# Optimization experiments

Measured on AMD Instinct MI355X. Metric: run time of the kernel, lower is better.

Reference implementation:

```python
import jax, jax.numpy as jnp
import numpy as np

N_NODES = 100000
N_EDGES = 3200000
OUT_CH = 128
X_DIM = 128


def setup_inputs() -> dict:
    key = jax.random.key(0)
    k1, k2, k3, k4 = jax.random.split(key, 4)
    x = jax.random.normal(k1, (N_NODES, X_DIM), dtype=jnp.float32)
    edge_index = jax.random.randint(k2, (2, N_EDGES), 0, N_NODES, dtype=jnp.int64)
    # torch nn.Linear(num_nodes, out_channels): weight [out, N], bias [out]
    W_weight = jax.random.normal(k3, (OUT_CH, N_NODES), dtype=jnp.float32) * (1.0 / np.sqrt(N_NODES))
    W_bias = jax.random.normal(k4, (OUT_CH,), dtype=jnp.float32) * 0.01
    return {"x": x, "edge_index": edge_index, "W_weight": W_weight, "W_bias": W_bias}


def reference(x, edge_index, W_weight, W_bias):
    """LINK forward: logits = A @ W.T + b, A = sparse COO adjacency from edge_index.

    A[r, c] = 1 for each edge (r, c), so row r of the output is
    sum_{c in neighbors(r)} W.T[c] + b  -> gather + segment_sum (SpMM).
    """
    N = x.shape[0]
    row, col = edge_index[0], edge_index[1]
    Wt = W_weight.T  # [N, out]
    gathered = Wt[col]  # [E, out] irregular gather
    logits = jax.ops.segment_sum(gathered, row, num_segments=N) + W_bias  # [N, out]
    return logits
```

## Files before the change

kernel.cpp:

```cpp
#include <hip/hip_runtime.h>
#include <hip/hip_bf16.h>


#define NCHUNK 256
#define RPB7 128
#define NB7 782
#define CAP 5120

__global__ __launch_bounds__(256) void absmax_kernel(const float* __restrict__ W,
                                                     int n4,
                                                     unsigned int* __restrict__ amax) {
    int i = blockIdx.x * blockDim.x + threadIdx.x;
    int stride = gridDim.x * blockDim.x;
    float m = 0.f;
    const float4* W4 = (const float4*)W;
    for (; i < n4; i += stride) {
        float4 v = W4[i];
        m = fmaxf(m, fmaxf(fmaxf(fabsf(v.x), fabsf(v.y)),
                           fmaxf(fabsf(v.z), fabsf(v.w))));
    }
    for (int off = 32; off > 0; off >>= 1) m = fmaxf(m, __shfl_xor(m, off));
    if ((threadIdx.x & 63) == 0) atomicMax(amax, __float_as_uint(m));
}

__global__ __launch_bounds__(256) void quant_kernel(const float* __restrict__ W,
                                                    unsigned char* __restrict__ Wt8,
                                                    const unsigned int* __restrict__ amax,
                                                    int N) {
    __shared__ float tile[128][33];
    int cx = threadIdx.x;
    int oy = threadIdx.y;
    int c = blockIdx.x * 32 + cx;
    for (int k = 0; k < 16; ++k) {
        int o = oy * 16 + k;
        tile[o][cx] = (c < N) ? W[(size_t)o * N + c] : 0.f;
    }
    __syncthreads();
    float M = __uint_as_float(*amax);
    float si = (M > 0.f) ? 127.f / M : 0.f;
    if (c < N) {
        unsigned int w[4];
#pragma unroll
        for (int d = 0; d < 4; ++d) {
            unsigned int acc = 0;
#pragma unroll
            for (int b = 0; b < 4; ++b) {
                int o = oy * 16 + d * 4 + b;
                int qi = __float2int_rn(tile[o][cx] * si) + 128;
                acc |= ((unsigned int)(qi & 0xff)) << (8 * b);
            }
            w[d] = acc;
        }
        *(uint4*)(Wt8 + (size_t)c * 128 + oy * 16) =
            make_uint4(w[0], w[1], w[2], w[3]);
    }
}

__global__ __launch_bounds__(1024) void p1_hist(const int* __restrict__ row,
                                                int E, int* __restrict__ hist) {
    __shared__ int lh[NB7];
    int b = blockIdx.x;
    for (int k = threadIdx.x; k < NB7; k += blockDim.x) lh[k] = 0;
    __syncthreads();
    int ch = (E + NCHUNK - 1) / NCHUNK;
    int s = b * ch, e = min(E, s + ch);
    for (int i = s + threadIdx.x; i < e; i += blockDim.x)
        atomicAdd(&lh[row[i] >> 7], 1);
    __syncthreads();
    for (int k = threadIdx.x; k < NB7; k += blockDim.x)
        hist[k * NCHUNK + b] = lh[k];
}

__global__ __launch_bounds__(256) void scan_sums(const int* __restrict__ v,
                                                 int* __restrict__ bsums, int M) {
    __shared__ int s[256];
    int i = blockIdx.x * 256 + threadIdx.x;
    s[threadIdx.x] = (i < M) ? v[i] : 0;
    __syncthreads();
    for (int off = 128; off > 0; off >>= 1) {
        if (threadIdx.x < off) s[threadIdx.x] += s[threadIdx.x + off];
        __syncthreads();
    }
    if (threadIdx.x == 0) bsums[blockIdx.x] = s[0];
}

__global__ __launch_bounds__(256) void scan_offsets_par(int* __restrict__ bsums,
                                                        int nb) {
    __shared__ int s[256];
    __shared__ int carry;
    if (threadIdx.x == 0) carry = 0;
    __syncthreads();
    for (int base = 0; base < nb; base += 256) {
        int i = base + threadIdx.x;
        int v = (i < nb) ? bsums[i] : 0;
        s[threadIdx.x] = v;
        __syncthreads();
        for (int off = 1; off < 256; off <<= 1) {
            int t = (threadIdx.x >= off) ? s[threadIdx.x - off] : 0;
            __syncthreads();
            s[threadIdx.x] += t;
            __syncthreads();
        }
        int incl = s[threadIdx.x];
        int c = carry;
        __syncthreads();
        if (threadIdx.x == 255) carry = c + incl;
        if (i < nb) bsums[i] = c + incl - v;
        __syncthreads();
    }
}

__global__ __launch_bounds__(256) void scan_finalT(const int* __restrict__ hist,
                                                   const int* __restrict__ bsums,
                                                   int* __restrict__ S_T,
                                                   int* __restrict__ bstart,
                                                   int M) {
    __shared__ int s[256];
    int i = blockIdx.x * 256 + threadIdx.x;
    int x = (i < M) ? hist[i] : 0;
    s[threadIdx.x] = x;
    __syncthreads();
    for (int off = 1; off < 256; off <<= 1) {
        int t = (threadIdx.x >= off) ? s[threadIdx.x - off] : 0;
        __syncthreads();
        s[threadIdx.x] += t;
        __syncthreads();
    }
    if (i < M) {
        int val = bsums[blockIdx.x] + s[threadIdx.x] - x;
        int k = i >> 8;
        int b = i & (NCHUNK - 1);
        S_T[(size_t)b * NB7 + k] = val;
        if (b == 0) bstart[k] = val;
    }
}

__global__ __launch_bounds__(1024) void p1_scatter(const int* __restrict__ row,
                                                   const int* __restrict__ col,
                                                   int E,
                                                   const int* __restrict__ S_T,
                                                   unsigned* __restrict__ packed) {
    __shared__ int lc[NB7];
    int b = blockIdx.x;
    const int* Srow = S_T + (size_t)b * NB7;
    for (int k = threadIdx.x; k < NB7; k += blockDim.x) lc[k] = Srow[k];
    __syncthreads();
    int ch = (E + NCHUNK - 1) / NCHUNK;
    int s = b * ch, e = min(E, s + ch);
    for (int i = s + threadIdx.x; i < e; i += blockDim.x) {
        int r = row[i], c = col[i];
        int p = atomicAdd(&lc[r >> 7], 1);
        packed[p] = ((unsigned)(r & 127) << 17) | (unsigned)c;
    }
}

__global__ __launch_bounds__(1024) void spmm_fused(
    const unsigned* __restrict__ packed, const int* __restrict__ bstart,
    const unsigned char* __restrict__ Wt8, const float* __restrict__ bias,
    const unsigned int* __restrict__ amax, float* __restrict__ out, int E,
    int N) {
    __shared__ unsigned g2[CAP];
    __shared__ int rhist[RPB7];
    __shared__ int rs[RPB7 + 1];
    __shared__ int cursor[RPB7];
    __shared__ int sscan[RPB7];
    int k = blockIdx.x;
    int start = bstart[k];
    int end = (k + 1 < NB7) ? bstart[k + 1] : E;
    int cnt = end - start;
    if (cnt > CAP) cnt = CAP;

    int tid = threadIdx.x;
    if (tid < RPB7) rhist[tid] = 0;
    __syncthreads();

    unsigned st0 = 0, st1 = 0, st2 = 0, st3 = 0, st4 = 0;
    {
        int i;
        i = tid;
        if (i < cnt) { st0 = packed[start + i]; atomicAdd(&rhist[st0 >> 17], 1); }
        i = tid + 1024;
        if (i < cnt) { st1 = packed[start + i]; atomicAdd(&rhist[st1 >> 17], 1); }
        i = tid + 2048;
        if (i < cnt) { st2 = packed[start + i]; atomicAdd(&rhist[st2 >> 17], 1); }
        i = tid + 3072;
        if (i < cnt) { st3 = packed[start + i]; atomicAdd(&rhist[st3 >> 17], 1); }
        i = tid + 4096;
        if (i < cnt) { st4 = packed[start + i]; atomicAdd(&rhist[st4 >> 17], 1); }
    }
    __syncthreads();
    {
        int v = 0;
        if (tid < RPB7) { v = rhist[tid]; sscan[tid] = v; }
        __syncthreads();
        for (int off = 1; off < RPB7; off <<= 1) {
            int t = 0;
            if (tid < RPB7 && tid >= off) t = sscan[tid - off];
            __syncthreads();
            if (tid < RPB7 && tid >= off) sscan[tid] += t;
            __syncthreads();
        }
        if (tid < RPB7) {
            rs[tid] = sscan[tid] - v;
            cursor[tid] = sscan[tid] - v;
            if (tid == RPB7 - 1) rs[RPB7] = sscan[RPB7 - 1];
        }
    }
    __syncthreads();
    {
        int i;
        i = tid;
        if (i < cnt) { int p = atomicAdd(&cursor[st0 >> 17], 1); g2[p] = (st0 & 0x1FFFFu) << 7; }
        i = tid + 1024;
        if (i < cnt) { int p = atomicAdd(&cursor[st1 >> 17], 1); g2[p] = (st1 & 0x1FFFFu) << 7; }
        i = tid + 2048;
        if (i < cnt) { int p = atomicAdd(&cursor[st2 >> 17], 1); g2[p] = (st2 & 0x1FFFFu) << 7; }
        i = tid + 3072;
        if (i < cnt) { int p = atomicAdd(&cursor[st3 >> 17], 1); g2[p] = (st3 & 0x1FFFFu) << 7; }
        i = tid + 4096;
        if (i < cnt) { int p = atomicAdd(&cursor[st4 >> 17], 1); g2[p] = (st4 & 0x1FFFFu) << 7; }
    }
    __syncthreads();

    float sg = __uint_as_float(*amax) / 127.f;
    int wave = tid >> 6, lane = tid & 63;
    int h = lane >> 5;
    int lane4 = (lane & 31) * 4;

    for (int ri = 0; ri < 8; ++ri) {
        int r = wave * 8 + ri;
        int gr = k * RPB7 + r;
        int js = rs[r], je = rs[r + 1];
        int m = je - js;
        int T = m >> 1;
        unsigned accA = 0, accB = 0;
        int idx = js + h;
        int t = 0;
        for (; t + 4 <= T; t += 4) {
            unsigned e0 = g2[idx + 0];
            unsigned e1 = g2[idx + 2];
            unsigned e2 = g2[idx + 4];
            unsigned e3 = g2[idx + 6];
            idx += 8;
            uint32_t u0 = *(const uint32_t*)(Wt8 + e0 + lane4);
            uint32_t u1 = *(const uint32_t*)(Wt8 + e1 + lane4);
            uint32_t u2 = *(const uint32_t*)(Wt8 + e2 + lane4);
            uint32_t u3 = *(const uint32_t*)(Wt8 + e3 + lane4);
            accA += (u0 & 0x00FF00FFu);
            accB += ((u0 >> 8) & 0x00FF00FFu);
            accA += (u1 & 0x00FF00FFu);
            accB += ((u1 >> 8) & 0x00FF00FFu);
            accA += (u2 & 0x00FF00FFu);
            accB += ((u2 >> 8) & 0x00FF00FFu);
            accA += (u3 & 0x00FF00FFu);
            accB += ((u3 >> 8) & 0x00FF00FFu);
        }
        for (; t < T; ++t) {
            unsigned e0 = g2[idx];
            idx += 2;
            uint32_t u0 = *(const uint32_t*)(Wt8 + e0 + lane4);
            accA += (u0 & 0x00FF00FFu);
            accB += ((u0 >> 8) & 0x00FF00FFu);
        }
        if ((m & 1) && h == 0) {
            unsigned e0 = g2[je - 1];
            uint32_t u0 = *(const uint32_t*)(Wt8 + e0 + lane4);
            accA += (u0 & 0x00FF00FFu);
            accB += ((u0 >> 8) & 0x00FF00FFu);
        }
        accA += __shfl_xor(accA, 32);
        accB += __shfl_xor(accB, 32);
        if (h == 0 && gr < N) {
            float fm = -128.f * (float)m;
            float4 b4 = *(const float4*)(bias + lane4);
            float4 res;
            res.x = fmaf(sg, (float)(accA & 0xffffu) + fm, b4.x);
            res.y = fmaf(sg, (float)(accB & 0xffffu) + fm, b4.y);
            res.z = fmaf(sg, (float)(accA >> 16) + fm, b4.z);
            res.w = fmaf(sg, (float)(accB >> 16) + fm, b4.w);
            *(float4*)(out + (size_t)gr * 128 + lane4) = res;
        }
    }
}

extern "C" void kernel_launch(void* const* d_in, const int* in_sizes, int n_in,
                              void* d_out, int out_size, void* d_ws,
                              size_t ws_size, hipStream_t stream) {
    const int* edge = (const int*)d_in[1];
    const float* W = (const float*)d_in[2];
    const float* bias = (const float*)d_in[3];
    float* out = (float*)d_out;

    const int N = in_sizes[0] / 128;
    const int E = in_sizes[1] / 2;
    const int* row = edge;
    const int* col = edge + E;

    const int M = NB7 * NCHUNK;
    const int nb1 = (M + 255) / 256;

    auto align16 = [](size_t v) { return (v + 15) & ~(size_t)15; };
    char* ws = (char*)d_ws;
    size_t off = 0;
    unsigned char* Wt8 = (unsigned char*)(ws + off);
    off = align16(off + (size_t)N * 128);
    unsigned* packed = (unsigned*)(ws + off);
    off = align16(off + (size_t)E * sizeof(unsigned));
    int* hist = (int*)(ws + off);
    off = align16(off + (size_t)M * sizeof(int));
    int* S_T = (int*)(ws + off);
    off = align16(off + (size_t)M * sizeof(int));
    int* bs1 = (int*)(ws + off);
    off = align16(off + (size_t)nb1 * sizeof(int));
    int* bstart = (int*)(ws + off);
    off = align16(off + (size_t)(NB7 + 1) * sizeof(int));
    unsigned int* amax = (unsigned int*)(ws + off);
    off = align16(off + 16);

    hipMemsetAsync(amax, 0, sizeof(unsigned int), stream);

    absmax_kernel<<<1024, 256, 0, stream>>>(W, (128 * N) / 4, amax);
    {
        dim3 block(32, 8);
        dim3 grid((N + 31) / 32);
        quant_kernel<<<grid, block, 0, stream>>>(W, Wt8, amax, N);
    }
    p1_hist<<<NCHUNK, 1024, 0, stream>>>(row, E, hist);
    scan_sums<<<nb1, 256, 0, stream>>>(hist, bs1, M);
    scan_offsets_par<<<1, 256, 0, stream>>>(bs1, nb1);
    scan_finalT<<<nb1, 256, 0, stream>>>(hist, bs1, S_T, bstart, M);
    p1_scatter<<<NCHUNK, 1024, 0, stream>>>(row, col, E, S_T, packed);
    spmm_fused<<<NB7, 1024, 0, stream>>>(packed, bstart, Wt8, bias, amax, out,
                                         E, N);
}
```

Measured before the change: 189.5 us.

## Split fused bin-sort SpMM into global row-sort pass and fine-grained gather kernel

The single fused kernel, which sorted each 128-row bin in shared memory and then gathered, is replaced by two kernels. A row-sort pass over coarser 512-row bins writes a full CSR (row starts plus column offsets) to global memory. A separate gather kernel with small 256-thread blocks then walks each row, broadcasting column indices across the wave with shuffles. The aim is higher occupancy and better latency hiding in the gather, and removing the shared-memory CAP limit. The cost is an extra kernel launch and an extra global write and read of the edge array.

New measurement: 204.0 us. 1.08x slower.

```diff
diff --git a/kernel.cpp b/kernel.cpp
--- a/kernel.cpp
+++ b/kernel.cpp
@@ -3,9 +3,8 @@
 
 
 #define NCHUNK 256
-#define RPB7 128
-#define NB7 782
-#define CAP 5120
+#define BINROWS 512
+#define NBIN 196
 
 __global__ __launch_bounds__(256) void absmax_kernel(const float* __restrict__ W,
                                                      int n4,
@@ -58,16 +57,16 @@
 
 __global__ __launch_bounds__(1024) void p1_hist(const int* __restrict__ row,
                                                 int E, int* __restrict__ hist) {
-    __shared__ int lh[NB7];
+    __shared__ int lh[NBIN];
     int b = blockIdx.x;
-    for (int k = threadIdx.x; k < NB7; k += blockDim.x) lh[k] = 0;
+    for (int k = threadIdx.x; k < NBIN; k += blockDim.x) lh[k] = 0;
     __syncthreads();
     int ch = (E + NCHUNK - 1) / NCHUNK;
     int s = b * ch, e = min(E, s + ch);
     for (int i = s + threadIdx.x; i < e; i += blockDim.x)
-        atomicAdd(&lh[row[i] >> 7], 1);
-    __syncthreads();
-    for (int k = threadIdx.x; k < NB7; k += blockDim.x)
+        atomicAdd(&lh[row[i] >> 9], 1);
+    __syncthreads();
+    for (int k = threadIdx.x; k < NBIN; k += blockDim.x)
         hist[k * NCHUNK + b] = lh[k];
 }
 
@@ -113,7 +112,7 @@
 __global__ __launch_bounds__(256) void scan_finalT(const int* __restrict__ hist,
                                                    const int* __restrict__ bsums,
                                                    int* __restrict__ S_T,
-                                                   int* __restrict__ bstart,
+                                                   int* __restrict__ binstart,
                                                    int M) {
     __shared__ int s[256];
     int i = blockIdx.x * 256 + threadIdx.x;
@@ -130,8 +129,8 @@
         int val = bsums[blockIdx.x] + s[threadIdx.x] - x;
         int k = i >> 8;
         int b = i & (NCHUNK - 1);
-        S_T[(size_t)b * NB7 + k] = val;
-        if (b == 0) bstart[k] = val;
+        S_T[(size_t)b * NBIN + k] = val;
+        if (b == 0) binstart[k] = val;
     }
 }
 
@@ -140,137 +139,108 @@
                                                    int E,
                                                    const int* __restrict__ S_T,
                                                    unsigned* __restrict__ packed) {
-    __shared__ int lc[NB7];
+    __shared__ int lc[NBIN];
     int b = blockIdx.x;
-    const int* Srow = S_T + (size_t)b * NB7;
-    for (int k = threadIdx.x; k < NB7; k += blockDim.x) lc[k] = Srow[k];
+    const int* Srow = S_T + (size_t)b * NBIN;
+    for (int k = threadIdx.x; k < NBIN; k += blockDim.x) lc[k] = Srow[k];
     __syncthreads();
     int ch = (E + NCHUNK - 1) / NCHUNK;
     int s = b * ch, e = min(E, s + ch);
     for (int i = s + threadIdx.x; i < e; i += blockDim.x) {
         int r = row[i], c = col[i];
-        int p = atomicAdd(&lc[r >> 7], 1);
-        packed[p] = ((unsigned)(r & 127) << 17) | (unsigned)c;
-    }
-}
-
-__global__ __launch_bounds__(1024) void spmm_fused(
-    const unsigned* __restrict__ packed, const int* __restrict__ bstart,
+        int p = atomicAdd(&lc[r >> 9], 1);
+        packed[p] = ((unsigned)(r & 511) << 17) | (unsigned)c;
+    }
+}
+
+__global__ __launch_bounds__(1024) void p2_rowsort(const unsigned* __restrict__ packed,
+                                                   const int* __restrict__ binstart,
+                                                   unsigned* __restrict__ colsorted,
+                                                   int* __restrict__ rowstart,
+                                                   int E) {
+    __shared__ int lh[BINROWS];
+    __shared__ int sc[BINROWS];
+    __shared__ int cur[BINROWS];
+    int b = blockIdx.x;
+    int tid = threadIdx.x;
+    int start = binstart[b];
+    int end = (b + 1 < NBIN) ? binstart[b + 1] : E;
+    if (tid < BINROWS) lh[tid] = 0;
+    __syncthreads();
+    for (int i = start + tid; i < end; i += 1024)
+        atomicAdd(&lh[packed[i] >> 17], 1);
+    __syncthreads();
+    int v = 0;
+    if (tid < BINROWS) { v = lh[tid]; sc[tid] = v; }
+    __syncthreads();
+    for (int off = 1; off < BINROWS; off <<= 1) {
+        int t = 0;
+        if (tid < BINROWS && tid >= off) t = sc[tid - off];
+        __syncthreads();
+        if (tid < BINROWS && tid >= off) sc[tid] += t;
+        __syncthreads();
+    }
+    if (tid < BINROWS) {
+        int excl = sc[tid] - v;
+        rowstart[b * BINROWS + tid] = start + excl;
+        cur[tid] = start + excl;
+    }
+    __syncthreads();
+    for (int i = start + tid; i < end; i += 1024) {
+        unsigned e2 = packed[i];
+        int p = atomicAdd(&cur[e2 >> 17], 1);
+        colsorted[p] = (e2 & 0x1FFFFu) << 7;
+    }
+}
+
+__global__ __launch_bounds__(256, 8) void spmm_gather(
+    const unsigned* __restrict__ colsorted, const int* __restrict__ rowstart,
     const unsigned char* __restrict__ Wt8, const float* __restrict__ bias,
-    const unsigned int* __restrict__ amax, float* __restrict__ out, int E,
-    int N) {
-    __shared__ unsigned g2[CAP];
-    __shared__ int rhist[RPB7];
-    __shared__ int rs[RPB7 + 1];
-    __shared__ int cursor[RPB7];
-    __shared__ int sscan[RPB7];
-    int k = blockIdx.x;
-    int start = bstart[k];
-    int end = (k + 1 < NB7) ? bstart[k + 1] : E;
-    int cnt = end - start;
-    if (cnt > CAP) cnt = CAP;
-
-    int tid = threadIdx.x;
-    if (tid < RPB7) rhist[tid] = 0;
-    __syncthreads();
-
-    unsigned st0 = 0, st1 = 0, st2 = 0, st3 = 0, st4 = 0;
-    {
-        int i;
-        i = tid;
-        if (i < cnt) { st0 = packed[start + i]; atomicAdd(&rhist[st0 >> 17], 1); }
-        i = tid + 1024;
-        if (i < cnt) { st1 = packed[start + i]; atomicAdd(&rhist[st1 >> 17], 1); }
-        i = tid + 2048;
-        if (i < cnt) { st2 = packed[start + i]; atomicAdd(&rhist[st2 >> 17], 1); }
-        i = tid + 3072;
-        if (i < cnt) { st3 = packed[start + i]; atomicAdd(&rhist[st3 >> 17], 1); }
-        i = tid + 4096;
-        if (i < cnt) { st4 = packed[start + i]; atomicAdd(&rhist[st4 >> 17], 1); }
-    }
-    __syncthreads();
-    {
-        int v = 0;
-        if (tid < RPB7) { v = rhist[tid]; sscan[tid] = v; }
-        __syncthreads();
-        for (int off = 1; off < RPB7; off <<= 1) {
-            int t = 0;
-            if (tid < RPB7 && tid >= off) t = sscan[tid - off];
-            __syncthreads();
-            if (tid < RPB7 && tid >= off) sscan[tid] += t;
-            __syncthreads();
-        }
-        if (tid < RPB7) {
-            rs[tid] = sscan[tid] - v;
-            cursor[tid] = sscan[tid] - v;
-            if (tid == RPB7 - 1) rs[RPB7] = sscan[RPB7 - 1];
-        }
-    }
-    __syncthreads();
-    {
-        int i;
-        i = tid;
-        if (i < cnt) { int p = atomicAdd(&cursor[st0 >> 17], 1); g2[p] = (st0 & 0x1FFFFu) << 7; }
-        i = tid + 1024;
-        if (i < cnt) { int p = atomicAdd(&cursor[st1 >> 17], 1); g2[p] = (st1 & 0x1FFFFu) << 7; }
-        i = tid + 2048;
-        if (i < cnt) { int p = atomicAdd(&cursor[st2 >> 17], 1); g2[p] = (st2 & 0x1FFFFu) << 7; }
-        i = tid + 3072;
-        if (i < cnt) { int p = atomicAdd(&cursor[st3 >> 17], 1); g2[p] = (st3 & 0x1FFFFu) << 7; }
-        i = tid + 4096;
-        if (i < cnt) { int p = atomicAdd(&cursor[st4 >> 17], 1); g2[p] = (st4 & 0x1FFFFu) << 7; }
-    }
-    __syncthreads();
-
+    const unsigned int* __restrict__ amax, float* __restrict__ out, int N) {
     float sg = __uint_as_float(*amax) / 127.f;
-    int wave = tid >> 6, lane = tid & 63;
+    int wave = threadIdx.x >> 6, lane = threadIdx.x & 63;
     int h = lane >> 5;
     int lane4 = (lane & 31) * 4;
 
-    for (int ri = 0; ri < 8; ++ri) {
-        int r = wave * 8 + ri;
-        int gr = k * RPB7 + r;
-        int js = rs[r], je = rs[r + 1];
+    int r0 = blockIdx.x * 16 + wave * 4;
+    for (int ri = 0; ri < 4; ++ri) {
+        int r = r0 + ri;
+        if (r >= N) return;
+        int js = rowstart[r], je = rowstart[r + 1];
         int m = je - js;
-        int T = m >> 1;
         unsigned accA = 0, accB = 0;
-        int idx = js + h;
-        int t = 0;
-        for (; t + 4 <= T; t += 4) {
-            unsigned e0 = g2[idx + 0];
-            unsigned e1 = g2[idx + 2];
-            unsigned e2 = g2[idx + 4];
-            unsigned e3 = g2[idx + 6];
-            idx += 8;
-            uint32_t u0 = *(const uint32_t*)(Wt8 + e0 + lane4);
-            uint32_t u1 = *(const uint32_t*)(Wt8 + e1 + lane4);
-            uint32_t u2 = *(const uint32_t*)(Wt8 + e2 + lane4);
-            uint32_t u3 = *(const uint32_t*)(Wt8 + e3 + lane4);
-            accA += (u0 & 0x00FF00FFu);
-            accB += ((u0 >> 8) & 0x00FF00FFu);
-            accA += (u1 & 0x00FF00FFu);
-            accB += ((u1 >> 8) & 0x00FF00FFu);
-            accA += (u2 & 0x00FF00FFu);
-            accB += ((u2 >> 8) & 0x00FF00FFu);
-            accA += (u3 & 0x00FF00FFu);
-            accB += ((u3 >> 8) & 0x00FF00FFu);
-        }
-        for (; t < T; ++t) {
-            unsigned e0 = g2[idx];
-            idx += 2;
-            uint32_t u0 = *(const uint32_t*)(Wt8 + e0 + lane4);
-            accA += (u0 & 0x00FF00FFu);
-            accB += ((u0 >> 8) & 0x00FF00FFu);
-        }
-        if ((m & 1) && h == 0) {
-            unsigned e0 = g2[je - 1];
-            uint32_t u0 = *(const uint32_t*)(Wt8 + e0 + lane4);
-            accA += (u0 & 0x00FF00FFu);
-            accB += ((u0 >> 8) & 0x00FF00FFu);
+        for (int base = js; base < je; base += 64) {
+            int nb = min(64, je - base);
+            unsigned cbs = (base + lane < je) ? colsorted[base + lane] : 0;
+            int T = nb >> 1;
+            int t = 0;
+            for (; t + 8 <= T; t += 8) {
+#pragma unroll
+                for (int u = 0; u < 8; ++u) {
+                    unsigned cb = __shfl(cbs, 2 * (t + u) + h);
+                    uint32_t w = *(const uint32_t*)(Wt8 + cb + lane4);
+                    accA += w & 0x00FF00FFu;
+                    accB += (w >> 8) & 0x00FF00FFu;
+                }
+            }
+            for (; t < T; ++t) {
+                unsigned cb = __shfl(cbs, 2 * t + h);
+                uint32_t w = *(const uint32_t*)(Wt8 + cb + lane4);
+                accA += w & 0x00FF00FFu;
+                accB += (w >> 8) & 0x00FF00FFu;
+            }
+            if (nb & 1) {
+                unsigned cb = __shfl(cbs, nb - 1);
+                if (h == 0) {
+                    uint32_t w = *(const uint32_t*)(Wt8 + cb + lane4);
+                    accA += w & 0x00FF00FFu;
+                    accB += (w >> 8) & 0x00FF00FFu;
+                }
+            }
         }
         accA += __shfl_xor(accA, 32);
         accB += __shfl_xor(accB, 32);
-        if (h == 0 && gr < N) {
+        if (h == 0) {
             float fm = -128.f * (float)m;
             float4 b4 = *(const float4*)(bias + lane4);
             float4 res;
@@ -278,7 +248,7 @@
             res.y = fmaf(sg, (float)(accB & 0xffffu) + fm, b4.y);
             res.z = fmaf(sg, (float)(accA >> 16) + fm, b4.z);
             res.w = fmaf(sg, (float)(accB >> 16) + fm, b4.w);
-            *(float4*)(out + (size_t)gr * 128 + lane4) = res;
+            *(float4*)(out + (size_t)r * 128 + lane4) = res;
         }
     }
 }
@@ -296,7 +266,7 @@
     const int* row = edge;
     const int* col = edge + E;
 
-    const int M = NB7 * NCHUNK;
+    const int M = NBIN * NCHUNK;
     const int nb1 = (M + 255) / 256;
 
     auto align16 = [](size_t v) { return (v + 15) & ~(size_t)15; };
@@ -306,14 +276,18 @@
     off = align16(off + (size_t)N * 128);
     unsigned* packed = (unsigned*)(ws + off);
     off = align16(off + (size_t)E * sizeof(unsigned));
+    unsigned* colsorted = (unsigned*)(ws + off);
+    off = align16(off + (size_t)E * sizeof(unsigned));
     int* hist = (int*)(ws + off);
     off = align16(off + (size_t)M * sizeof(int));
     int* S_T = (int*)(ws + off);
     off = align16(off + (size_t)M * sizeof(int));
     int* bs1 = (int*)(ws + off);
     off = align16(off + (size_t)nb1 * sizeof(int));
-    int* bstart = (int*)(ws + off);
-    off = align16(off + (size_t)(NB7 + 1) * sizeof(int));
+    int* binstart = (int*)(ws + off);
+    off = align16(off + (size_t)(NBIN + 1) * sizeof(int));
+    int* rowstart = (int*)(ws + off);
+    off = align16(off + (size_t)(NBIN * BINROWS + 1) * sizeof(int));
     unsigned int* amax = (unsigned int*)(ws + off);
     off = align16(off + 16);
 
@@ -328,8 +302,10 @@
     p1_hist<<<NCHUNK, 1024, 0, stream>>>(row, E, hist);
     scan_sums<<<nb1, 256, 0, stream>>>(hist, bs1, M);
     scan_offsets_par<<<1, 256, 0, stream>>>(bs1, nb1);
-    scan_finalT<<<nb1, 256, 0, stream>>>(hist, bs1, S_T, bstart, M);
+    scan_finalT<<<nb1, 256, 0, stream>>>(hist, bs1, S_T, binstart, M);
     p1_scatter<<<NCHUNK, 1024, 0, stream>>>(row, col, E, S_T, packed);
-    spmm_fused<<<NB7, 1024, 0, stream>>>(packed, bstart, Wt8, bias, amax, out,
-                                         E, N);
-}
+    p2_rowsort<<<NBIN, 1024, 0, stream>>>(packed, binstart, colsorted, rowstart,
+                                          E);
+    spmm_gather<<<(N + 15) / 16, 256, 0, stream>>>(colsorted, rowstart, Wt8,
+                                                   bias, amax, out, N);
+}
```
